# Optimization experiments

Measured on AMD Instinct MI355X. Metric: run time of the kernel, lower is better.

Reference implementation:

```python
import jax, jax.numpy as jnp
import numpy as np

B, L, H, S = 8, 2048, 8, 128


def setup_inputs() -> dict:
    key = jax.random.key(0)
    k1, k2, k3 = jax.random.split(key, 3)
    x = jax.random.normal(k1, (B, L, S), dtype=jnp.float32)
    W = jax.random.normal(k2, (L, H), dtype=jnp.float32)          # per-head Toeplitz logits, W[j, h] fills diagonal -j
    A = jax.random.normal(k3, (H * S, H * S), dtype=jnp.float32)  # bilinear form for stage-2 attention
    return {"x": x, "W": W, "A": A}


def reference(x, W, A):
    Bb, Ll, Ss = x.shape
    Hh = W.shape[1]
    HS = Hh * Ss
    # Stage 1: causal Toeplitz softmax attention per head.
    # Original fills diagonal -j of W_h with W[j, h], masks strictly-upper with -inf, softmaxes rows.
    d = jnp.arange(Ll)[:, None] - jnp.arange(Ll)[None, :]          # (L, L), i - j
    logits = jnp.where(d[..., None] >= 0,
                       W[jnp.clip(d, 0, Ll - 1)],                  # (L, L, H), W[i-j, h] on valid band
                       -jnp.inf)
    P = jax.nn.softmax(logits, axis=1)                             # softmax over key axis j
    attn = jnp.einsum('ijh,bjs->bihs', P, x).reshape(Bb, Ll, HS)   # heads concatenated
    X1 = jnp.concatenate([attn, x], axis=-1)                       # (B, L, (H+1)*S)
    # Stage 2: single-query bilinear attention from last token over previous tokens.
    q = X1[:, -1, :HS]                                             # (B, HS)
    keys = X1[:, :-1, :HS]                                         # (B, L-1, HS)
    scores = jnp.einsum('bd,de,ble->bl', q, A, keys)               # (B, L-1)
    w2 = jax.nn.softmax(scores, axis=-1)
    # values are the raw-x slice X1[:, :-1, HS:] == x[:, :-1, :]
    out = jnp.einsum('bl,bls->bs', w2, x[:, :-1, :])               # (B, S)
    return out
```

## Files before the change

kernel.cpp:

```cpp
#include <hip/hip_runtime.h>

#define L 2048
#define H 8
#define S 128
#define B 8
#define HS 1024

__global__ __launch_bounds__(512) void kA_prep_qpart(const float* __restrict__ W,
                                                     const float* __restrict__ x,
                                                     float* __restrict__ Eb,
                                                     float* __restrict__ Zb,
                                                     float* __restrict__ partial_q,
                                                     unsigned* __restrict__ counters) {
  const int b = blockIdx.x, jc = blockIdx.y;
  const int t = threadIdx.x;
  if (b == 0 && jc == 0 && t < 8) counters[t] = 0u;

  __shared__ float ew[128][H];
  __shared__ float part[16][H][S];
  __shared__ float tot[512];

  const int base = jc * 128;
  const int dhi = L - 1 - base;
#pragma unroll
  for (int k = 0; k < 2; ++k) {
    const int idx = t + k * 512;
    const int i = idx >> 3, h = idx & 7;
    ew[i][h] = expf(W[(size_t)(dhi - i) * H + h]);
  }

  if (jc < H) {
    const int h = jc;
    const int d0 = t * 4;
    float e[4];
    float run = 0.f;
#pragma unroll
    for (int k = 0; k < 4; ++k) {
      float v = expf(W[(size_t)(d0 + k) * H + h]);
      e[k] = v; run += v;
    }
    tot[t] = run;
    __syncthreads();
    for (int off = 1; off < 512; off <<= 1) {
      float v = (t >= off) ? tot[t - off] : 0.f;
      __syncthreads();
      tot[t] += v;
      __syncthreads();
    }
    float c = (t == 0) ? 0.f : tot[t - 1];
    const size_t ebase = (size_t)(b * H + h) * L;
#pragma unroll
    for (int k = 0; k < 4; ++k) {
      c += e[k];
      Eb[ebase + d0 + k] = e[k];
      Zb[ebase + d0 + k] = c;
    }
  }
  __syncthreads();

  const int s4 = t & 31;
  const int r = t >> 5;
  const float4* __restrict__ x4 = (const float4*)(x + (size_t)b * L * S);
  float4 acc[H];
#pragma unroll
  for (int h = 0; h < H; ++h) acc[h] = make_float4(0.f, 0.f, 0.f, 0.f);
#pragma unroll
  for (int k = 0; k < 8; ++k) {
    const int ll = k * 16 + r;
    const int l = base + ll;
    const float4 xv = x4[(size_t)l * 32 + s4];
#pragma unroll
    for (int h = 0; h < H; ++h) {
      const float w = ew[ll][h];
      acc[h].x += w * xv.x; acc[h].y += w * xv.y;
      acc[h].z += w * xv.z; acc[h].w += w * xv.w;
    }
  }
#pragma unroll
  for (int h = 0; h < H; ++h) {
    part[r][h][s4 * 4 + 0] = acc[h].x;
    part[r][h][s4 * 4 + 1] = acc[h].y;
    part[r][h][s4 * 4 + 2] = acc[h].z;
    part[r][h][s4 * 4 + 3] = acc[h].w;
  }
  __syncthreads();
#pragma unroll
  for (int k = 0; k < 2; ++k) {
    const int idx = t + k * 512;
    const int h = idx >> 7, s = idx & 127;
    float sm = 0.f;
#pragma unroll
    for (int rr = 0; rr < 16; ++rr) sm += part[rr][h][s];
    partial_q[((size_t)b * 16 + jc) * HS + idx] = sm;
  }
}

__global__ __launch_bounds__(512) void kB_v(const float* __restrict__ partial_q,
                                            const float* __restrict__ Zb,
                                            const float* __restrict__ A,
                                            float* __restrict__ partial_v) {
  const int ebase = blockIdx.x * 128;
  const int dc = blockIdx.y;
  const int dbase = dc * 64;
  const int t = threadIdx.x;
  __shared__ float ql[8][64];
  __shared__ float p2[4][8][128];
  const float invZ = 1.f / Zb[(size_t)(dc >> 1) * L + (L - 1)];
  {
    const int bb = t >> 6, dl = t & 63;
    const float* __restrict__ pq = partial_q + ((size_t)bb * 16) * HS + dbase + dl;
    float a0 = 0.f, a1 = 0.f, a2 = 0.f, a3 = 0.f;
#pragma unroll
    for (int j4 = 0; j4 < 16; j4 += 4) {
      a0 += pq[(size_t)(j4 + 0) * HS];
      a1 += pq[(size_t)(j4 + 1) * HS];
      a2 += pq[(size_t)(j4 + 2) * HS];
      a3 += pq[(size_t)(j4 + 3) * HS];
    }
    ql[bb][dl] = ((a0 + a1) + (a2 + a3)) * invZ;
  }
  __syncthreads();
  const int el = t & 127, dg = t >> 7;
  const int e = ebase + el;
  const float* __restrict__ Ab = A + (size_t)(dbase + dg * 16) * HS + e;
  float acc[8] = {0.f, 0.f, 0.f, 0.f, 0.f, 0.f, 0.f, 0.f};
#pragma unroll 4
  for (int dd = 0; dd < 16; ++dd) {
    const float a = Ab[(size_t)dd * HS];
    const int d = dg * 16 + dd;
    acc[0] += ql[0][d] * a;
    acc[1] += ql[1][d] * a;
    acc[2] += ql[2][d] * a;
    acc[3] += ql[3][d] * a;
    acc[4] += ql[4][d] * a;
    acc[5] += ql[5][d] * a;
    acc[6] += ql[6][d] * a;
    acc[7] += ql[7][d] * a;
  }
#pragma unroll
  for (int bb = 0; bb < 8; ++bb) p2[dg][bb][el] = acc[bb];
  __syncthreads();
#pragma unroll
  for (int k = 0; k < 2; ++k) {
    const int idx = t + k * 512;
    const int bb = idx >> 7, el2 = idx & 127;
    partial_v[((size_t)bb * 16 + dc) * HS + ebase + el2] =
        (p2[0][bb][el2] + p2[1][bb][el2]) + (p2[2][bb][el2] + p2[3][bb][el2]);
  }
}

__global__ __launch_bounds__(512) void kC_u(const float* __restrict__ x,
                                            const float* __restrict__ partial_v,
                                            float* __restrict__ u_pad) {
  const int b = blockIdx.x, jc = blockIdx.y;
  const int t = threadIdx.x;
  __shared__ float vs[HS];
  __shared__ float up[4][H][128];
#pragma unroll
  for (int k = 0; k < 2; ++k) {
    const int i = t + k * 512;
    float a0 = 0.f, a1 = 0.f, a2 = 0.f, a3 = 0.f;
#pragma unroll
    for (int dcc = 0; dcc < 16; dcc += 4) {
      a0 += partial_v[((size_t)b * 16 + dcc + 0) * HS + i];
      a1 += partial_v[((size_t)b * 16 + dcc + 1) * HS + i];
      a2 += partial_v[((size_t)b * 16 + dcc + 2) * HS + i];
      a3 += partial_v[((size_t)b * 16 + dcc + 3) * HS + i];
    }
    vs[i] = (a0 + a1) + (a2 + a3);
  }
  __syncthreads();
  const int jl = t & 127, sq = t >> 7;
  const int j = jc * 128 + jl;
  const float4* __restrict__ xr = (const float4*)(x + ((size_t)b * L + j) * S) + sq * 8;
  float4 xv[8];
#pragma unroll
  for (int i = 0; i < 8; ++i) xv[i] = xr[i];
  float acc[H];
#pragma unroll
  for (int h = 0; h < H; ++h) {
    const float4* __restrict__ vv = (const float4*)(vs + h * S + sq * 32);
    float a = 0.f;
#pragma unroll
    for (int i = 0; i < 8; ++i) {
      const float4 w = vv[i];
      a += xv[i].x * w.x + xv[i].y * w.y + xv[i].z * w.z + xv[i].w * w.w;
    }
    acc[h] = a;
  }
#pragma unroll
  for (int h = 0; h < H; ++h) up[sq][h][jl] = acc[h];
  __syncthreads();
#pragma unroll
  for (int k = 0; k < 2; ++k) {
    const int idx = t + k * 512;
    const int h = idx >> 7, j2 = idx & 127;
    const float sv = (up[0][h][j2] + up[1][h][j2]) + (up[2][h][j2] + up[3][h][j2]);
    const size_t rowbase = (size_t)(b * H + h) * (2 * L);
    u_pad[rowbase + jc * 128 + j2] = 0.f;
    u_pad[rowbase + L + jc * 128 + j2] = sv;
  }
}

__global__ __launch_bounds__(512) void kD_conv(const float* __restrict__ u_pad,
                                               const float* __restrict__ Eb,
                                               const float* __restrict__ Zb,
                                               float* __restrict__ partial_s) {
  const int b = blockIdx.x;
  const int rr = blockIdx.y;
  int lt = 0, c = 0;
  while (c + (lt / 2 + 1) <= rr) { c += lt / 2 + 1; ++lt; }
  const int dtt = rr - c;
  const int l0 = lt * 128;
  const int t = threadIdx.x;
  const int tsub = t & 31;
  const int h = (t >> 5) & 7;
  const int dh = t >> 8;

  __shared__ float u_win[H][512];
  __shared__ float sred[2][H][128];

  const int w0 = l0 - dtt * 256 - 384;
#pragma unroll
  for (int k = 0; k < 2; ++k) {
    const int idx = t + k * 512;
    const int hh = idx >> 7, i4 = idx & 127;
    const float4 v = *(const float4*)(u_pad + (size_t)(b * H + hh) * (2 * L) + L + w0 + i4 * 4);
    *(float4*)&u_win[hh][i4 * 4] = v;
  }
  __syncthreads();

  const int dbase = dtt * 256 + dh * 128;
  const int Lb = l0 + tsub * 4;
  const int lb0 = tsub * 4 - dh * 128 + 376;
  const float4* __restrict__ Eh4 = (const float4*)(Eb + (size_t)(b * H + h) * L);
  float acc0 = 0.f, acc1 = 0.f, acc2 = 0.f, acc3 = 0.f;
  float4 lo = *(const float4*)&u_win[h][lb0 + 4];
  float4 hi = *(const float4*)&u_win[h][lb0 + 8];
#pragma unroll 4
  for (int dd = 0; dd < 128; dd += 4) {
    const int d0 = dbase + dd;
    const float4 ev  = Eh4[d0 >> 2];
    const float4 nlo = *(const float4*)&u_win[h][lb0 - dd];
    acc0 += ev.x * hi.x; acc1 += ev.x * hi.y; acc2 += ev.x * hi.z; acc3 += ev.x * hi.w;
    acc0 += ev.y * lo.w; acc1 += ev.y * hi.x; acc2 += ev.y * hi.y; acc3 += ev.y * hi.z;
    acc0 += ev.z * lo.z; acc1 += ev.z * lo.w; acc2 += ev.z * hi.x; acc3 += ev.z * hi.y;
    acc0 += ev.w * lo.y; acc1 += ev.w * lo.z; acc2 += ev.w * lo.w; acc3 += ev.w * hi.x;
    hi = lo; lo = nlo;
  }
  const float4 zv = *(const float4*)&Zb[(size_t)(b * H + h) * L + Lb];
  sred[dh][h][tsub * 4 + 0] = acc0 / zv.x;
  sred[dh][h][tsub * 4 + 1] = acc1 / zv.y;
  sred[dh][h][tsub * 4 + 2] = acc2 / zv.z;
  sred[dh][h][tsub * 4 + 3] = acc3 / zv.w;
  __syncthreads();
  if (t < 128) {
    float sc = 0.f;
#pragma unroll
    for (int hh = 0; hh < H; ++hh) sc += sred[0][hh][t] + sred[1][hh][t];
    partial_s[((size_t)b * 8 + dtt) * L + l0 + t] = sc;
  }
}

__global__ __launch_bounds__(512) void kF_out(const float* __restrict__ x,
                                              const float* __restrict__ partial_s,
                                              float* __restrict__ partial,
                                              unsigned* __restrict__ counters,
                                              float* __restrict__ out) {
  const int b = blockIdx.x, c = blockIdx.y;
  const int t = threadIdx.x;
  __shared__ float ep[L];
  __shared__ float red[512];
  __shared__ float part[16][S];

  const int l0 = t * 4;
  const int ltq = t >> 6;
  float sc[4] = {0.f, 0.f, 0.f, 0.f};
  for (int dtt = 0; dtt <= ltq; ++dtt) {
    const float4 a = *(const float4*)(partial_s + ((size_t)b * 8 + dtt) * L + l0);
    sc[0] += a.x; sc[1] += a.y; sc[2] += a.z; sc[3] += a.w;
  }
  if (t == 511) sc[3] = -3.4e38f;
  float mx = fmaxf(fmaxf(sc[0], sc[1]), fmaxf(sc[2], sc[3]));
  red[t] = mx;
  __syncthreads();
  for (int off = 256; off > 0; off >>= 1) {
    if (t < off) red[t] = fmaxf(red[t], red[t + off]);
    __syncthreads();
  }
  mx = red[0];
  __syncthreads();
  float e[4];
  float sm = 0.f;
#pragma unroll
  for (int k = 0; k < 4; ++k) {
    e[k] = (l0 + k < L - 1) ? expf(sc[k] - mx) : 0.f;
    sm += e[k];
  }
  red[t] = sm;
  __syncthreads();
  for (int off = 256; off > 0; off >>= 1) {
    if (t < off) red[t] += red[t + off];
    __syncthreads();
  }
  const float inv = 1.f / red[0];
#pragma unroll
  for (int k = 0; k < 4; ++k) ep[l0 + k] = e[k] * inv;
  __syncthreads();

  const int s4 = t & 31;
  const int r = t >> 5;
  const int base = c * 128;
  const float4* __restrict__ x4 = (const float4*)(x + (size_t)b * L * S);
  float4 acc = make_float4(0.f, 0.f, 0.f, 0.f);
#pragma unroll
  for (int k = 0; k < 8; ++k) {
    const int l = base + k * 16 + r;
    const float w = ep[l];
    const float4 xv = x4[(size_t)l * 32 + s4];
    acc.x += w * xv.x; acc.y += w * xv.y; acc.z += w * xv.z; acc.w += w * xv.w;
  }
  part[r][s4 * 4 + 0] = acc.x;
  part[r][s4 * 4 + 1] = acc.y;
  part[r][s4 * 4 + 2] = acc.z;
  part[r][s4 * 4 + 3] = acc.w;
  __syncthreads();
  if (t < S) {
    float smv = 0.f;
#pragma unroll
    for (int rr = 0; rr < 16; ++rr) smv += part[rr][t];
    partial[((size_t)b * 16 + c) * S + t] = smv;
  }
  __threadfence();
  __syncthreads();
  __shared__ unsigned lastFlag;
  if (t == 0)
    lastFlag = (atomicAdd(&counters[0], 1u) == (unsigned)(B * 16 - 1)) ? 1u : 0u;
  __syncthreads();
  if (lastFlag) {
#pragma unroll
    for (int k = 0; k < 2; ++k) {
      const int idx = t + k * 512;
      const int b2 = idx >> 7, s = idx & 127;
      float a = 0.f;
#pragma unroll 4
      for (int cc = 0; cc < 16; ++cc) a += partial[((size_t)b2 * 16 + cc) * S + s];
      out[b2 * S + s] = a;
    }
  }
}

extern "C" void kernel_launch(void* const* d_in, const int* in_sizes, int n_in,
                              void* d_out, int out_size, void* d_ws, size_t ws_size,
                              hipStream_t stream) {
  const float* x = (const float*)d_in[0];
  const float* W = (const float*)d_in[1];
  const float* A = (const float*)d_in[2];
  float* out = (float*)d_out;

  float* ws        = (float*)d_ws;
  float* Eb        = ws;
  float* Zb        = Eb + (size_t)B * H * L;
  float* partial_q = Zb + (size_t)B * H * L;
  float* partial_v = partial_q + (size_t)B * 16 * HS;
  float* u_pad     = partial_v + (size_t)B * 16 * HS;
  float* partial_s = u_pad + (size_t)B * H * 2 * L;
  float* partial   = partial_s + (size_t)B * 8 * L;
  unsigned* counters = (unsigned*)(partial + (size_t)B * 16 * S);

  kA_prep_qpart<<<dim3(B, 16), 512, 0, stream>>>(W, x, Eb, Zb, partial_q, counters);
  kB_v         <<<dim3(8, 16), 512, 0, stream>>>(partial_q, Zb, A, partial_v);
  kC_u         <<<dim3(B, 16), 512, 0, stream>>>(x, partial_v, u_pad);
  kD_conv      <<<dim3(B, 72), 512, 0, stream>>>(u_pad, Eb, Zb, partial_s);
  kF_out       <<<dim3(B, 16), 512, 0, stream>>>(x, partial_s, partial, counters, out);
}
```

Before: 52.06 us.

## Fuse u computation into convolution kernel and drop u_pad buffer

Removes the separate kC_u kernel and its u_pad intermediate. Each kD_conv block now reduces partial_v into shared memory and computes its own 512-wide u window directly from x, with zeros for negative indices. This saves one launch and a global write/read round trip. The cost is redundant work: across the 72 blocks per batch the partial_v reduction and the x·v dot products are recomputed many times, because overlapping windows are produced independently.

```diff
diff --git a/kernel.cpp b/kernel.cpp
--- a/kernel.cpp
+++ b/kernel.cpp
@@ -149,60 +149,8 @@
   }
 }
 
-__global__ __launch_bounds__(512) void kC_u(const float* __restrict__ x,
-                                            const float* __restrict__ partial_v,
-                                            float* __restrict__ u_pad) {
-  const int b = blockIdx.x, jc = blockIdx.y;
-  const int t = threadIdx.x;
-  __shared__ float vs[HS];
-  __shared__ float up[4][H][128];
-#pragma unroll
-  for (int k = 0; k < 2; ++k) {
-    const int i = t + k * 512;
-    float a0 = 0.f, a1 = 0.f, a2 = 0.f, a3 = 0.f;
-#pragma unroll
-    for (int dcc = 0; dcc < 16; dcc += 4) {
-      a0 += partial_v[((size_t)b * 16 + dcc + 0) * HS + i];
-      a1 += partial_v[((size_t)b * 16 + dcc + 1) * HS + i];
-      a2 += partial_v[((size_t)b * 16 + dcc + 2) * HS + i];
-      a3 += partial_v[((size_t)b * 16 + dcc + 3) * HS + i];
-    }
-    vs[i] = (a0 + a1) + (a2 + a3);
-  }
-  __syncthreads();
-  const int jl = t & 127, sq = t >> 7;
-  const int j = jc * 128 + jl;
-  const float4* __restrict__ xr = (const float4*)(x + ((size_t)b * L + j) * S) + sq * 8;
-  float4 xv[8];
-#pragma unroll
-  for (int i = 0; i < 8; ++i) xv[i] = xr[i];
-  float acc[H];
-#pragma unroll
-  for (int h = 0; h < H; ++h) {
-    const float4* __restrict__ vv = (const float4*)(vs + h * S + sq * 32);
-    float a = 0.f;
-#pragma unroll
-    for (int i = 0; i < 8; ++i) {
-      const float4 w = vv[i];
-      a += xv[i].x * w.x + xv[i].y * w.y + xv[i].z * w.z + xv[i].w * w.w;
-    }
-    acc[h] = a;
-  }
-#pragma unroll
-  for (int h = 0; h < H; ++h) up[sq][h][jl] = acc[h];
-  __syncthreads();
-#pragma unroll
-  for (int k = 0; k < 2; ++k) {
-    const int idx = t + k * 512;
-    const int h = idx >> 7, j2 = idx & 127;
-    const float sv = (up[0][h][j2] + up[1][h][j2]) + (up[2][h][j2] + up[3][h][j2]);
-    const size_t rowbase = (size_t)(b * H + h) * (2 * L);
-    u_pad[rowbase + jc * 128 + j2] = 0.f;
-    u_pad[rowbase + L + jc * 128 + j2] = sv;
-  }
-}
-
-__global__ __launch_bounds__(512) void kD_conv(const float* __restrict__ u_pad,
+__global__ __launch_bounds__(512) void kD_conv(const float* __restrict__ x,
+                                               const float* __restrict__ partial_v,
                                                const float* __restrict__ Eb,
                                                const float* __restrict__ Zb,
                                                float* __restrict__ partial_s) {
@@ -217,17 +165,52 @@
   const int h = (t >> 5) & 7;
   const int dh = t >> 8;
 
+  __shared__ float vs[HS];
   __shared__ float u_win[H][512];
   __shared__ float sred[2][H][128];
 
+#pragma unroll
+  for (int k = 0; k < 2; ++k) {
+    const int i = t + k * 512;
+    float a0 = 0.f, a1 = 0.f, a2 = 0.f, a3 = 0.f;
+#pragma unroll
+    for (int dcc = 0; dcc < 16; dcc += 4) {
+      a0 += partial_v[((size_t)b * 16 + dcc + 0) * HS + i];
+      a1 += partial_v[((size_t)b * 16 + dcc + 1) * HS + i];
+      a2 += partial_v[((size_t)b * 16 + dcc + 2) * HS + i];
+      a3 += partial_v[((size_t)b * 16 + dcc + 3) * HS + i];
+    }
+    vs[i] = (a0 + a1) + (a2 + a3);
+  }
+  __syncthreads();
+
   const int w0 = l0 - dtt * 256 - 384;
-#pragma unroll
-  for (int k = 0; k < 2; ++k) {
-    const int idx = t + k * 512;
-    const int hh = idx >> 7, i4 = idx & 127;
-    const float4 v = *(const float4*)(u_pad + (size_t)(b * H + hh) * (2 * L) + L + w0 + i4 * 4);
-    *(float4*)&u_win[hh][i4 * 4] = v;
-  }
+  const int j = w0 + t;
+  float uacc[H];
+#pragma unroll
+  for (int hh = 0; hh < H; ++hh) uacc[hh] = 0.f;
+  if (j >= 0) {
+    const float4* __restrict__ xr = (const float4*)(x + ((size_t)b * L + j) * S);
+#pragma unroll
+    for (int sc4 = 0; sc4 < 32; sc4 += 8) {
+      float4 xv[8];
+#pragma unroll
+      for (int i = 0; i < 8; ++i) xv[i] = xr[sc4 + i];
+#pragma unroll
+      for (int hh = 0; hh < H; ++hh) {
+        const float4* __restrict__ vv = (const float4*)(vs + hh * S) + sc4;
+        float a = 0.f;
+#pragma unroll
+        for (int i = 0; i < 8; ++i) {
+          const float4 w = vv[i];
+          a += xv[i].x * w.x + xv[i].y * w.y + xv[i].z * w.z + xv[i].w * w.w;
+        }
+        uacc[hh] += a;
+      }
+    }
+  }
+#pragma unroll
+  for (int hh = 0; hh < H; ++hh) u_win[hh][t] = uacc[hh];
   __syncthreads();
 
   const int dbase = dtt * 256 + dh * 128;
@@ -363,14 +346,12 @@
   float* Zb        = Eb + (size_t)B * H * L;
   float* partial_q = Zb + (size_t)B * H * L;
   float* partial_v = partial_q + (size_t)B * 16 * HS;
-  float* u_pad     = partial_v + (size_t)B * 16 * HS;
-  float* partial_s = u_pad + (size_t)B * H * 2 * L;
+  float* partial_s = partial_v + (size_t)B * 16 * HS;
   float* partial   = partial_s + (size_t)B * 8 * L;
   unsigned* counters = (unsigned*)(partial + (size_t)B * 16 * S);
 
   kA_prep_qpart<<<dim3(B, 16), 512, 0, stream>>>(W, x, Eb, Zb, partial_q, counters);
   kB_v         <<<dim3(8, 16), 512, 0, stream>>>(partial_q, Zb, A, partial_v);
-  kC_u         <<<dim3(B, 16), 512, 0, stream>>>(x, partial_v, u_pad);
-  kD_conv      <<<dim3(B, 72), 512, 0, stream>>>(u_pad, Eb, Zb, partial_s);
+  kD_conv      <<<dim3(B, 72), 512, 0, stream>>>(x, partial_v, Eb, Zb, partial_s);
   kF_out       <<<dim3(B, 16), 512, 0, stream>>>(x, partial_s, partial, counters, out);
 }
```

After: 76.24 us. 1.46x slower.
